# Kernel optimization log

Hardware: AMD Instinct MI355X
Metric: run time of the kernel (lower is better)

Reference implementation:

```python
import jax, jax.numpy as jnp
import numpy as np

GAMMA = 1.0   # focal exponent
THETA = 1.0   # boundary weight scale
SIGMA = 1.0   # distance decay
EPS = 1e-8
BIG = 1e10    # 'no boundary point in this column' sentinel


def _boundary(mask):
    # mask: [H,W] bool. Boundary = foreground pixel with a 4-neighbor background
    # (image border counts as background via zero padding).
    p = jnp.pad(mask, 1)
    inner = (p[1:-1, 1:-1] & p[:-2, 1:-1] & p[2:, 1:-1]
             & p[1:-1, :-2] & p[1:-1, 2:])
    return mask & ~inner


def _sqdist(mask):
    # Exact squared Euclidean distance transform to the True pixels of mask,
    # via separable two-pass min:  d2(x,y) = min_{y'} [ (y-y')^2 + min_{x':mask[x',y']} (x-x')^2 ]
    H, W = mask.shape
    xs = jnp.arange(H, dtype=jnp.float32)
    dx2 = (xs[:, None] - xs[None, :]) ** 2                      # [H,H]
    col = jnp.where(mask, 0.0, BIG)                             # [H,W]
    g = jnp.min(dx2[:, :, None] + col[None, :, :], axis=1)      # [H,W] min over x'
    ys = jnp.arange(W, dtype=jnp.float32)
    dy2 = (ys[:, None] - ys[None, :]) ** 2                      # [W,W] (y,y')
    return jnp.min(g[:, None, :] + dy2[None, :, :], axis=2)     # [H,W] min over y'


def _weight_map(prob, label):
    # prob, label: [H,W] float
    ib = _boundary(prob > 0.5)    # predicted-image boundary pixels
    lb = _boundary(label > 0.5)   # label boundary pixels
    d_to_ib = jnp.sqrt(_sqdist(ib))   # distance of every pixel to nearest image boundary
    d_to_lb = jnp.sqrt(_sqdist(lb))   # distance of every pixel to nearest label boundary
    w = (1.0
         + THETA * jnp.where(lb, jnp.exp(-d_to_ib / SIGMA), 0.0)
         + THETA * jnp.where(ib, jnp.exp(-d_to_lb / SIGMA), 0.0))
    return w


def setup_inputs() -> dict:
    key = jax.random.key(0)
    k1, k2 = jax.random.split(key)
    B, H, W = 8, 256, 256
    inp = jax.random.normal(k1, (B, H, W), dtype=jnp.float32)
    target = (jax.random.uniform(k2, (B, H, W)) < 0.5).astype(jnp.float32)
    return {"input": inp, "target": target}


def reference(input, target):
    probs = jax.nn.sigmoid(input)
    # weight maps are built from detached CPU copies in the original -> stop_gradient
    w = jax.lax.stop_gradient(jax.vmap(_weight_map)(probs, target))
    loss = w * (-(1.0 - probs) ** GAMMA * target * jnp.log(probs + EPS)
                - probs ** GAMMA * (1.0 - target) * jnp.log(1.0 - probs + EPS))
    return jnp.mean(loss)
```

## Files before the change

kernel.cpp:

```cpp
#include <hip/hip_runtime.h>

#define HW_BIG   1e10f
#define LOSS_EPS 1e-8f

typedef unsigned long long u64;

__device__ __forceinline__ int row_nearest(const u64* rm, int y) {
    const int yw = y >> 6, yb = y & 63;
    int dd = 32768;
    u64 w = rm[yw] & (~0ULL >> (63 - yb));
    int j = yw;
    while (w == 0 && j > 0) w = rm[--j];
    if (w) dd = y - (j * 64 + 63 - __builtin_clzll(w));
    u64 w2 = rm[yw] & (~0ULL << yb);
    int j2 = yw;
    while (w2 == 0 && j2 < 3) w2 = rm[++j2];
    if (w2) { int du = (j2 * 64 + __builtin_ctzll(w2)) - y; dd = min(dd, du); }
    return dd;
}

__global__ void k_masks(const float* __restrict__ inp,
                        const float* __restrict__ tgt,
                        u64* __restrict__ mv,
                        u64* __restrict__ ml) {
    const size_t gid = (size_t)blockIdx.x * 256 + threadIdx.x;
    const bool vb = inp[gid] > 0.0f;
    const bool tb = tgt[gid] > 0.5f;
    const u64 bv = __ballot(vb);
    const u64 bt = __ballot(tb);
    if ((threadIdx.x & 63) == 0) {
        mv[gid >> 6] = bv;
        ml[gid >> 6] = bt;
    }
}

__global__ void k_dt_loss(const float* __restrict__ inp,
                          const u64* __restrict__ mv,
                          const u64* __restrict__ ml,
                          float* __restrict__ partials) {
    __shared__ u64 Mv[1024];
    __shared__ u64 Ml[1024];
    __shared__ u64 Bib[1024];
    __shared__ u64 Blb[1024];
    __shared__ float G1[256][8];
    __shared__ float G2[256][8];
    __shared__ float wsum[16];
    const int tid = threadIdx.x;
    const int img = blockIdx.x >> 5;
    const int y0  = (blockIdx.x & 31) * 8;
    const int x   = tid >> 2;
    const int yq  = tid & 3;
    const int ya  = y0 + yq;
    const int yb  = ya + 4;

    const size_t mbase = (size_t)img * 1024;
    Mv[tid] = mv[mbase + tid];
    Ml[tid] = ml[mbase + tid];
    const float va = inp[((size_t)img * 256 + x) * 256 + ya];
    const float vb = inp[((size_t)img * 256 + x) * 256 + yb];
    __syncthreads();

    {
        const int xr_ = tid >> 2, j = tid & 3;
        u64 own = Mv[tid];
        u64 up  = (xr_ > 0)   ? Mv[tid - 4] : 0ULL;
        u64 dn  = (xr_ < 255) ? Mv[tid + 4] : 0ULL;
        u64 lf  = (own << 1) | ((j > 0) ? (Mv[tid - 1] >> 63) : 0ULL);
        u64 rt  = (own >> 1) | ((j < 3) ? (Mv[tid + 1] << 63) : 0ULL);
        Bib[tid] = own & ~(up & dn & lf & rt);
        own = Ml[tid];
        up  = (xr_ > 0)   ? Ml[tid - 4] : 0ULL;
        dn  = (xr_ < 255) ? Ml[tid + 4] : 0ULL;
        lf  = (own << 1) | ((j > 0) ? (Ml[tid - 1] >> 63) : 0ULL);
        rt  = (own >> 1) | ((j < 3) ? (Ml[tid + 1] << 63) : 0ULL);
        Blb[tid] = own & ~(up & dn & lf & rt);
    }
    __syncthreads();

    const int ywa = ya >> 6, yba = ya & 63;
    const int ywb = yb >> 6, ybb = yb & 63;
    const bool fibA = (Bib[x * 4 + ywa] >> yba) & 1;
    const bool flbA = (Blb[x * 4 + ywa] >> yba) & 1;
    const float tA  = ((Ml[x * 4 + ywa] >> yba) & 1) ? 1.0f : 0.0f;
    const bool fibB = (Bib[x * 4 + ywb] >> ybb) & 1;
    const bool flbB = (Blb[x * 4 + ywb] >> ybb) & 1;
    const float tB  = ((Ml[x * 4 + ywb] >> ybb) & 1) ? 1.0f : 0.0f;

    {
        const int d1a = row_nearest(&Bib[x * 4], ya);
        const int d2a = row_nearest(&Blb[x * 4], ya);
        const int d1b = row_nearest(&Bib[x * 4], yb);
        const int d2b = row_nearest(&Blb[x * 4], yb);
        G1[x][yq]     = (d1a > 255) ? HW_BIG : (float)(d1a * d1a);
        G2[x][yq]     = (d2a > 255) ? HW_BIG : (float)(d2a * d2a);
        G1[x][yq + 4] = (d1b > 255) ? HW_BIG : (float)(d1b * d1b);
        G2[x][yq + 4] = (d2b > 255) ? HW_BIG : (float)(d2b * d2b);
    }
    __syncthreads();

    float m1a = flbA ? G1[x][yq] : 0.0f;
    float m2a = fibA ? G2[x][yq] : 0.0f;
    for (int d = 1; d < 256; ++d) {
        const float fd2 = (float)(d * d);
        if (fd2 >= m1a && fd2 >= m2a) break;
        const int xl = x - d;
        if (xl >= 0)  { m1a = fminf(m1a, G1[xl][yq] + fd2); m2a = fminf(m2a, G2[xl][yq] + fd2); }
        const int xr = x + d;
        if (xr < 256) { m1a = fminf(m1a, G1[xr][yq] + fd2); m2a = fminf(m2a, G2[xr][yq] + fd2); }
    }
    float m1b = flbB ? G1[x][yq + 4] : 0.0f;
    float m2b = fibB ? G2[x][yq + 4] : 0.0f;
    for (int d = 1; d < 256; ++d) {
        const float fd2 = (float)(d * d);
        if (fd2 >= m1b && fd2 >= m2b) break;
        const int xl = x - d;
        if (xl >= 0)  { m1b = fminf(m1b, G1[xl][yq + 4] + fd2); m2b = fminf(m2b, G2[xl][yq + 4] + fd2); }
        const int xr = x + d;
        if (xr < 256) { m1b = fminf(m1b, G1[xr][yq + 4] + fd2); m2b = fminf(m2b, G2[xr][yq + 4] + fd2); }
    }

    const float pa = 1.0f / (1.0f + __expf(-va));
    float wA = 1.0f;
    if (flbA) wA += __expf(-sqrtf(m1a));
    if (fibA) wA += __expf(-sqrtf(m2a));
    float lossA = wA * (-(1.0f - pa) * tA * __logf(pa + LOSS_EPS)
                        - pa * (1.0f - tA) * __logf(1.0f - pa + LOSS_EPS));

    const float pb = 1.0f / (1.0f + __expf(-vb));
    float wB = 1.0f;
    if (flbB) wB += __expf(-sqrtf(m1b));
    if (fibB) wB += __expf(-sqrtf(m2b));
    float lossB = wB * (-(1.0f - pb) * tB * __logf(pb + LOSS_EPS)
                        - pb * (1.0f - tB) * __logf(1.0f - pb + LOSS_EPS));

    float s = lossA + lossB;
#pragma unroll
    for (int off = 32; off > 0; off >>= 1) s += __shfl_down(s, off, 64);
    if ((tid & 63) == 0) wsum[tid >> 6] = s;
    __syncthreads();
    if (tid == 0) {
        float bs = 0.0f;
#pragma unroll
        for (int i = 0; i < 16; ++i) bs += wsum[i];
        partials[blockIdx.x] = bs;
    }
}

__global__ void k_reduce(const float* __restrict__ partials, int n,
                         float* __restrict__ out, double inv_count) {
    __shared__ double sw[4];
    const int tid = threadIdx.x;
    double s = 0.0;
    for (int i = tid; i < n; i += 256) s += (double)partials[i];
#pragma unroll
    for (int off = 32; off > 0; off >>= 1) s += __shfl_down(s, off, 64);
    const int lane = tid & 63, wv = tid >> 6;
    if (lane == 0) sw[wv] = s;
    __syncthreads();
    if (tid == 0) out[0] = (float)(((sw[0] + sw[1]) + (sw[2] + sw[3])) * inv_count);
}

extern "C" void kernel_launch(void* const* d_in, const int* in_sizes, int n_in,
                              void* d_out, int out_size, void* d_ws, size_t ws_size,
                              hipStream_t stream) {
    const float* inp = (const float*)d_in[0];
    const float* tgt = (const float*)d_in[1];
    float* out = (float*)d_out;

    const int total = in_sizes[0];
    const int nimg  = total / 65536;
    const int nblk1 = total / 256;
    const int nblk2 = nimg * 32;

    char* ws = (char*)d_ws;
    u64*   mv    = (u64*)ws;
    u64*   ml    = mv + (size_t)nimg * 1024;
    float* parts = (float*)(ml + (size_t)nimg * 1024);

    k_masks  <<<nblk1, 256,  0, stream>>>(inp, tgt, mv, ml);
    k_dt_loss<<<nblk2, 1024, 0, stream>>>(inp, mv, ml, parts);
    k_reduce <<<1,     256,  0, stream>>>(parts, nblk2, out, 1.0 / (double)total);
}
```

Baseline: 17.35 us.

## Vectorize mask build, branchless row scan, merged unrolled column min loop

The mask kernel now loads float4 per thread and assembles 64-bit mask words with xor-shuffles, so it launches a quarter as many blocks. The row-nearest search runs branchlessly on the four mask words held in registers instead of looping over shared memory. The two boundary G arrays are interleaved into one padded float2 array, and the two column-min loops are merged into one loop unrolled by 4, using clamped indices and a single shared early-exit bound. This cuts divergence, shared-memory traffic and loop overhead, but each thread may do extra iterations until all four of its minima have converged.

Result: slower. 19.02 us (+9.6%).

```diff
diff --git a/kernel.cpp b/kernel.cpp
--- a/kernel.cpp
+++ b/kernel.cpp
@@ -5,32 +5,57 @@
 
 typedef unsigned long long u64;
 
-__device__ __forceinline__ int row_nearest(const u64* rm, int y) {
+__device__ __forceinline__ int row_nearest_reg(u64 w0, u64 w1, u64 w2, u64 w3,
+                                               int y) {
     const int yw = y >> 6, yb = y & 63;
-    int dd = 32768;
-    u64 w = rm[yw] & (~0ULL >> (63 - yb));
-    int j = yw;
-    while (w == 0 && j > 0) w = rm[--j];
-    if (w) dd = y - (j * 64 + 63 - __builtin_clzll(w));
-    u64 w2 = rm[yw] & (~0ULL << yb);
-    int j2 = yw;
-    while (w2 == 0 && j2 < 3) w2 = rm[++j2];
-    if (w2) { int du = (j2 * 64 + __builtin_ctzll(w2)) - y; dd = min(dd, du); }
-    return dd;
+    const u64 lowm  = (~0ULL) >> (63 - yb);
+    const u64 highm = (~0ULL) << yb;
+    u64 d0 = (yw == 0) ? (w0 & lowm) : w0;
+    u64 d1 = (yw < 1) ? 0ULL : ((yw == 1) ? (w1 & lowm) : w1);
+    u64 d2 = (yw < 2) ? 0ULL : ((yw == 2) ? (w2 & lowm) : w2);
+    u64 d3 = (yw < 3) ? 0ULL : ((yw == 3) ? (w3 & lowm) : w3);
+    int hb = -32768;
+    hb = d0 ? (63  - __builtin_clzll(d0)) : hb;
+    hb = d1 ? (127 - __builtin_clzll(d1)) : hb;
+    hb = d2 ? (191 - __builtin_clzll(d2)) : hb;
+    hb = d3 ? (255 - __builtin_clzll(d3)) : hb;
+    const int dn = y - hb;
+    u64 u0 = (yw == 0) ? (w0 & highm) : 0ULL;
+    u64 u1 = (yw == 1) ? (w1 & highm) : ((yw < 1) ? w1 : 0ULL);
+    u64 u2 = (yw == 2) ? (w2 & highm) : ((yw < 2) ? w2 : 0ULL);
+    u64 u3 = (yw == 3) ? (w3 & highm) : ((yw < 3) ? w3 : 0ULL);
+    int ls = 32768 + y;
+    ls = u3 ? (192 + (int)__builtin_ctzll(u3)) : ls;
+    ls = u2 ? (128 + (int)__builtin_ctzll(u2)) : ls;
+    ls = u1 ? (64  + (int)__builtin_ctzll(u1)) : ls;
+    ls = u0 ? ((int)__builtin_ctzll(u0))       : ls;
+    const int up = ls - y;
+    return min(dn, up);
 }
 
 __global__ void k_masks(const float* __restrict__ inp,
                         const float* __restrict__ tgt,
                         u64* __restrict__ mv,
                         u64* __restrict__ ml) {
-    const size_t gid = (size_t)blockIdx.x * 256 + threadIdx.x;
-    const bool vb = inp[gid] > 0.0f;
-    const bool tb = tgt[gid] > 0.5f;
-    const u64 bv = __ballot(vb);
-    const u64 bt = __ballot(tb);
-    if ((threadIdx.x & 63) == 0) {
-        mv[gid >> 6] = bv;
-        ml[gid >> 6] = bt;
+    const int t = threadIdx.x;
+    const size_t gid4 = (size_t)blockIdx.x * 256 + t;
+    const float4 v4 = reinterpret_cast<const float4*>(inp)[gid4];
+    const float4 t4 = reinterpret_cast<const float4*>(tgt)[gid4];
+    const unsigned nv = (unsigned)(v4.x > 0.0f) | ((unsigned)(v4.y > 0.0f) << 1)
+                      | ((unsigned)(v4.z > 0.0f) << 2) | ((unsigned)(v4.w > 0.0f) << 3);
+    const unsigned nt = (unsigned)(t4.x > 0.5f) | ((unsigned)(t4.y > 0.5f) << 1)
+                      | ((unsigned)(t4.z > 0.5f) << 2) | ((unsigned)(t4.w > 0.5f) << 3);
+    const int sh = (t & 15) * 4;
+    u64 wv_ = ((u64)nv) << sh;
+    u64 wt_ = ((u64)nt) << sh;
+#pragma unroll
+    for (int off = 1; off < 16; off <<= 1) {
+        wv_ |= (u64)__shfl_xor((long long)wv_, off, 64);
+        wt_ |= (u64)__shfl_xor((long long)wt_, off, 64);
+    }
+    if ((t & 15) == 0) {
+        mv[gid4 >> 4] = wv_;
+        ml[gid4 >> 4] = wt_;
     }
 }
 
@@ -42,8 +67,7 @@
     __shared__ u64 Ml[1024];
     __shared__ u64 Bib[1024];
     __shared__ u64 Blb[1024];
-    __shared__ float G1[256][8];
-    __shared__ float G2[256][8];
+    __shared__ float2 GG[256][10];
     __shared__ float wsum[16];
     const int tid = threadIdx.x;
     const int img = blockIdx.x >> 5;
@@ -51,13 +75,13 @@
     const int x   = tid >> 2;
     const int yq  = tid & 3;
     const int ya  = y0 + yq;
-    const int yb  = ya + 4;
+    const int yv  = ya + 4;
 
     const size_t mbase = (size_t)img * 1024;
     Mv[tid] = mv[mbase + tid];
     Ml[tid] = ml[mbase + tid];
     const float va = inp[((size_t)img * 256 + x) * 256 + ya];
-    const float vb = inp[((size_t)img * 256 + x) * 256 + yb];
+    const float vb = inp[((size_t)img * 256 + x) * 256 + yv];
     __syncthreads();
 
     {
@@ -77,46 +101,55 @@
     }
     __syncthreads();
 
-    const int ywa = ya >> 6, yba = ya & 63;
-    const int ywb = yb >> 6, ybb = yb & 63;
-    const bool fibA = (Bib[x * 4 + ywa] >> yba) & 1;
-    const bool flbA = (Blb[x * 4 + ywa] >> yba) & 1;
-    const float tA  = ((Ml[x * 4 + ywa] >> yba) & 1) ? 1.0f : 0.0f;
-    const bool fibB = (Bib[x * 4 + ywb] >> ybb) & 1;
-    const bool flbB = (Blb[x * 4 + ywb] >> ybb) & 1;
-    const float tB  = ((Ml[x * 4 + ywb] >> ybb) & 1) ? 1.0f : 0.0f;
-
-    {
-        const int d1a = row_nearest(&Bib[x * 4], ya);
-        const int d2a = row_nearest(&Blb[x * 4], ya);
-        const int d1b = row_nearest(&Bib[x * 4], yb);
-        const int d2b = row_nearest(&Blb[x * 4], yb);
-        G1[x][yq]     = (d1a > 255) ? HW_BIG : (float)(d1a * d1a);
-        G2[x][yq]     = (d2a > 255) ? HW_BIG : (float)(d2a * d2a);
-        G1[x][yq + 4] = (d1b > 255) ? HW_BIG : (float)(d1b * d1b);
-        G2[x][yq + 4] = (d2b > 255) ? HW_BIG : (float)(d2b * d2b);
-    }
-    __syncthreads();
-
-    float m1a = flbA ? G1[x][yq] : 0.0f;
-    float m2a = fibA ? G2[x][yq] : 0.0f;
-    for (int d = 1; d < 256; ++d) {
-        const float fd2 = (float)(d * d);
-        if (fd2 >= m1a && fd2 >= m2a) break;
-        const int xl = x - d;
-        if (xl >= 0)  { m1a = fminf(m1a, G1[xl][yq] + fd2); m2a = fminf(m2a, G2[xl][yq] + fd2); }
-        const int xr = x + d;
-        if (xr < 256) { m1a = fminf(m1a, G1[xr][yq] + fd2); m2a = fminf(m2a, G2[xr][yq] + fd2); }
-    }
-    float m1b = flbB ? G1[x][yq + 4] : 0.0f;
-    float m2b = fibB ? G2[x][yq + 4] : 0.0f;
-    for (int d = 1; d < 256; ++d) {
-        const float fd2 = (float)(d * d);
-        if (fd2 >= m1b && fd2 >= m2b) break;
-        const int xl = x - d;
-        if (xl >= 0)  { m1b = fminf(m1b, G1[xl][yq + 4] + fd2); m2b = fminf(m2b, G2[xl][yq + 4] + fd2); }
-        const int xr = x + d;
-        if (xr < 256) { m1b = fminf(m1b, G1[xr][yq + 4] + fd2); m2b = fminf(m2b, G2[xr][yq + 4] + fd2); }
+    const u64 b0 = Bib[x * 4 + 0], b1 = Bib[x * 4 + 1];
+    const u64 b2 = Bib[x * 4 + 2], b3 = Bib[x * 4 + 3];
+    const u64 l0 = Blb[x * 4 + 0], l1 = Blb[x * 4 + 1];
+    const u64 l2 = Blb[x * 4 + 2], l3 = Blb[x * 4 + 3];
+    const int yw = ya >> 6;
+    const u64 mlw = Ml[x * 4 + yw];
+    const int yba = ya & 63, ybb = yv & 63;
+    const u64 bw = (yw == 0) ? b0 : (yw == 1) ? b1 : (yw == 2) ? b2 : b3;
+    const u64 lw = (yw == 0) ? l0 : (yw == 1) ? l1 : (yw == 2) ? l2 : l3;
+    const bool fibA = (bw >> yba) & 1, fibB = (bw >> ybb) & 1;
+    const bool flbA = (lw >> yba) & 1, flbB = (lw >> ybb) & 1;
+    const float tA = ((mlw >> yba) & 1) ? 1.0f : 0.0f;
+    const float tB = ((mlw >> ybb) & 1) ? 1.0f : 0.0f;
+
+    const int d1a = row_nearest_reg(b0, b1, b2, b3, ya);
+    const int d2a = row_nearest_reg(l0, l1, l2, l3, ya);
+    const int d1b = row_nearest_reg(b0, b1, b2, b3, yv);
+    const int d2b = row_nearest_reg(l0, l1, l2, l3, yv);
+    const float g1a = (d1a > 255) ? HW_BIG : (float)(d1a * d1a);
+    const float g2a = (d2a > 255) ? HW_BIG : (float)(d2a * d2a);
+    const float g1b = (d1b > 255) ? HW_BIG : (float)(d1b * d1b);
+    const float g2b = (d2b > 255) ? HW_BIG : (float)(d2b * d2b);
+    GG[x][yq]     = make_float2(g1a, g2a);
+    GG[x][yq + 4] = make_float2(g1b, g2b);
+    __syncthreads();
+
+    float m1a = flbA ? g1a : 0.0f;
+    float m2a = fibA ? g2a : 0.0f;
+    float m1b = flbB ? g1b : 0.0f;
+    float m2b = fibB ? g2b : 0.0f;
+    float mm = fmaxf(fmaxf(m1a, m2a), fmaxf(m1b, m2b));
+    for (int d = 1; d < 256; d += 4) {
+        if ((float)(d * d) >= mm) break;
+#pragma unroll
+        for (int k = 0; k < 4; ++k) {
+            const int dd = d + k;
+            const float fd2 = (float)(dd * dd);
+            const int xl = (x - dd > 0) ? (x - dd) : 0;
+            const int xr = (x + dd < 255) ? (x + dd) : 255;
+            const float2 glA = GG[xl][yq];
+            const float2 grA = GG[xr][yq];
+            const float2 glB = GG[xl][yq + 4];
+            const float2 grB = GG[xr][yq + 4];
+            m1a = fminf(fminf(m1a, glA.x + fd2), grA.x + fd2);
+            m2a = fminf(fminf(m2a, glA.y + fd2), grA.y + fd2);
+            m1b = fminf(fminf(m1b, glB.x + fd2), grB.x + fd2);
+            m2b = fminf(fminf(m2b, glB.y + fd2), grB.y + fd2);
+        }
+        mm = fmaxf(fmaxf(m1a, m2a), fmaxf(m1b, m2b));
     }
 
     const float pa = 1.0f / (1.0f + __expf(-va));
@@ -169,7 +202,7 @@
 
     const int total = in_sizes[0];
     const int nimg  = total / 65536;
-    const int nblk1 = total / 256;
+    const int nblk1 = total / 1024;
     const int nblk2 = nimg * 32;
 
     char* ws = (char*)d_ws;
```
